# Kernel optimization log

Hardware: AMD Instinct MI355X
Metric: run time of the kernel (lower is better)

Reference implementation:

```python
import jax, jax.numpy as jnp
import numpy as np

MIN_DIST = 32  # minimum_extrema_distance from init_kwargs


def _extrema_mask(x):
    # x: [L]. Matches torch: dx padded with 0 on right (>0) and left (<=0);
    # sign = (1 - sign(x)).bool() is True iff x <= 0.
    dx = x[1:] - x[:-1]
    right = jnp.pad(dx, (0, 1)) > 0        # rising on the right
    left = jnp.pad(dx, (1, 0)) <= 0        # non-rising on the left
    neg = x <= 0
    valleys = right & left & neg
    peaks = (~right) & (~left) & (~neg)
    return valleys | peaks


def _suppress(x):
    # Greedy NMS-like suppression over one sample. x: [L]
    L = x.shape[0]
    e = _extrema_mask(x)
    # Sort ALL positions by |x| descending, with non-extrema pushed to the end
    key = jnp.where(e, jnp.abs(x), -jnp.inf)
    order = jnp.argsort(-key)              # candidate j -> original index order[j]
    valid = e[order]                       # which sorted candidates are real extrema
    idx = order                            # original positions, in sorted order

    def step(sec, i):
        # If candidate i not yet suppressed: suppress all candidates within
        # MIN_DIST of its position, then un-suppress itself.
        cond = jnp.logical_not(sec[i])
        window = (idx >= idx[i] - MIN_DIST) & (idx <= idx[i] + MIN_DIST)
        new_sec = jnp.where(cond, (sec | window).at[i].set(False), sec)
        return new_sec, None

    sec0 = jnp.logical_not(valid)          # non-extrema start suppressed
    sec, _ = jax.lax.scan(step, sec0, jnp.arange(L))
    primary_sorted = valid & jnp.logical_not(sec)
    # scatter back to original positions (order is a permutation)
    primary = jnp.zeros((L,), dtype=bool).at[order].set(primary_sorted)
    return jnp.where(primary, x, jnp.zeros_like(x))


def setup_inputs() -> dict:
    key = jax.random.key(0)
    input_ = jax.random.normal(key, (128, 1, 4096), dtype=jnp.float32)
    return {"input_": input_}


def reference(input_):
    x = input_[:, 0, :]                    # [B, L]
    out = jax.vmap(_suppress)(x)           # [B, L]
    return out[:, None, :]                 # [B, 1, L]
```

## Files before the change

kernel.cpp:

```cpp
#include <hip/hip_runtime.h>

#define L 4096
#define NT 256
#define C 16
#define NC (NT + 4)

typedef unsigned int u32;
typedef unsigned long long u64;

static __device__ __forceinline__ u32 umax(u32 a, u32 b) { return a > b ? a : b; }

__global__ __launch_bounds__(NT) void extrema_nms_kernel(const float* __restrict__ in,
                                                         float* __restrict__ out) {
    __shared__ u32 pfxT[C][NC];
    __shared__ u32 sfxT[C][NC];
    __shared__ u32 TA[NC];
    __shared__ u32 winmF[2 * NC];
    __shared__ int flagsF[2];

    const int tid = threadIdx.x;
    const int cc = tid + 2;
    const int base = tid * C;
    const float* xrow = in + (size_t)blockIdx.x * L;

    if (tid < 64) {
        int o = tid >> 2, c = tid & 3;
        int col = (c & 1) + ((c >> 1) ? (NT + 2) : 0);
        pfxT[o][col] = 0;
        sfxT[o][col] = 0;
    }
    if (tid < 2) { TA[tid] = 0; TA[NT + 2 + tid] = 0; }
    for (int w = tid; w < 2 * NC; w += NT) winmF[w] = 0;
    if (tid == 0) { flagsF[0] = 0; flagsF[1] = 0; }

    float xv[C];
    #pragma unroll
    for (int k = 0; k < C; k += 4) {
        float4 f = *reinterpret_cast<const float4*>(xrow + base + k);
        xv[k] = f.x; xv[k + 1] = f.y; xv[k + 2] = f.z; xv[k + 3] = f.w;
    }
    float xl = (base > 0) ? xrow[base - 1] : 0.0f;
    float xr = (base + C < L) ? xrow[base + C] : 0.0f;

    u32 key[C];
    #pragma unroll
    for (int o = 0; o < C; ++o) {
        int i = base + o;
        float xi = xv[o];
        float xp = (o == 0) ? xl : xv[o - 1];
        float xn = (o == C - 1) ? xr : xv[o + 1];
        bool right = (i < L - 1) && (xn > xi);
        bool left  = (i == 0) || (xi <= xp);
        bool neg   = (xi <= 0.0f);
        bool ext = (right && left && neg) || (!right && !left && !neg);
        key[o] = ext ? ((__float_as_uint(xi) & 0x7fffffffu) + 1u) : 0u;
    }

    u32 run = 0, om = 0;
    {
        u32 p = 0;
        #pragma unroll
        for (int o = 0; o < C; ++o) { p = umax(p, key[o]); pfxT[o][cc] = p; }
        TA[cc] = p;
        u32 s = 0;
        #pragma unroll
        for (int o = C - 1; o >= 0; --o) { s = umax(s, key[o]); sfxT[o][cc] = s; }
        #pragma unroll
        for (int o = 0; o < C; ++o) if (key[o] > run) { run = key[o]; om = (u32)o; }
    }
    u32 keptm = 0;
    __syncthreads();

    for (int r = 0; r < 200; ++r) {
        if (run) {
            u32 bL = umax(sfxT[om][cc - 2], TA[cc - 1]);
            u32 bR = umax(TA[cc + 1], pfxT[om][cc + 2]);
            u32 wm = (bL < run && bR <= run) ? (1u << om) : 0u;
            winmF[(r & 1) * NC + cc] = wm;
            if (wm) { keptm |= wm; flagsF[r & 1] = 1; }
        }
        __syncthreads();

        int go = flagsF[r & 1];
        const int pp = (r & 1) * NC;
        u32 m0 = winmF[pp + cc - 2], m1 = winmF[pp + cc - 1], m2 = winmF[pp + cc];
        u32 m3 = winmF[pp + cc + 1], m4 = winmF[pp + cc + 2];
        if (!go) break;
        if (tid == 0) flagsF[(r + 1) & 1] = 0;
        u64 W0 = (u64)(m0 & 0xffffu) | ((u64)(m1 & 0xffffu) << 16)
               | ((u64)(m2 & 0xffffu) << 32) | ((u64)(m3 & 0xffffu) << 48);
        u32 W1 = m4 & 0xffffu;
        u32 supmask = 0;
        if (W0) { int h0 = 63 - __clzll(W0); supmask = (u32)((2ULL << h0) - 1ULL); }
        if (W1) { int l1 = __ffs(W1) - 1;    supmask |= ~((1u << l1) - 1u); }
        supmask &= 0xffffu;
        if (run && supmask) {
            #pragma unroll
            for (int o = 0; o < C; ++o) if ((supmask >> o) & 1u) key[o] = 0;
            u32 p = 0;
            #pragma unroll
            for (int o = 0; o < C; ++o) { p = umax(p, key[o]); pfxT[o][cc] = p; }
            TA[cc] = p;
            u32 s = 0;
            #pragma unroll
            for (int o = C - 1; o >= 0; --o) { s = umax(s, key[o]); sfxT[o][cc] = s; }
            run = 0; om = 0;
            #pragma unroll
            for (int o = 0; o < C; ++o) if (key[o] > run) { run = key[o]; om = (u32)o; }
        }
        __syncthreads();
    }

    float* orow = out + (size_t)blockIdx.x * L;
    #pragma unroll
    for (int k = 0; k < C; k += 4) {
        float4 f;
        f.x = ((keptm >> (k + 0)) & 1u) ? xv[k + 0] : 0.0f;
        f.y = ((keptm >> (k + 1)) & 1u) ? xv[k + 1] : 0.0f;
        f.z = ((keptm >> (k + 2)) & 1u) ? xv[k + 2] : 0.0f;
        f.w = ((keptm >> (k + 3)) & 1u) ? xv[k + 3] : 0.0f;
        *reinterpret_cast<float4*>(orow + base + k) = f;
    }
}

extern "C" void kernel_launch(void* const* d_in, const int* in_sizes, int n_in,
                              void* d_out, int out_size, void* d_ws, size_t ws_size,
                              hipStream_t stream) {
    const float* in = (const float*)d_in[0];
    float* out = (float*)d_out;
    int rows = in_sizes[0] / L;
    extrema_nms_kernel<<<rows, NT, 0, stream>>>(in, out);
}
```

Baseline: 12.31 us.

## Transpose prefix/suffix tables to per-thread rows with vectorized shared stores

Moves the per-thread prefix and suffix max tables from column-major [C][NC] arrays to row-major per-thread rows padded to a stride of 20, so each thread writes its 16 values with four uint4 shared stores. The block total now lives in slot 16 of the prefix row instead of a separate array. It also fuses the argmax into the prefix scan, uses the thread's own window mask from a register instead of reloading it, and skips neighbour mask loads when the thread has no candidate. The padded stride is meant to limit bank conflicts, but neighbour reads at an index that varies per thread could still conflict.

```diff
diff --git a/kernel.cpp b/kernel.cpp
--- a/kernel.cpp
+++ b/kernel.cpp
@@ -4,6 +4,7 @@
 #define NT 256
 #define C 16
 #define NC (NT + 4)
+#define SS 20
 
 typedef unsigned int u32;
 typedef unsigned long long u64;
@@ -12,9 +13,8 @@
 
 __global__ __launch_bounds__(NT) void extrema_nms_kernel(const float* __restrict__ in,
                                                          float* __restrict__ out) {
-    __shared__ u32 pfxT[C][NC];
-    __shared__ u32 sfxT[C][NC];
-    __shared__ u32 TA[NC];
+    __shared__ u32 pfxS[NC * SS];
+    __shared__ u32 sfxS[NC * SS];
     __shared__ u32 winmF[2 * NC];
     __shared__ int flagsF[2];
 
@@ -23,14 +23,18 @@
     const int base = tid * C;
     const float* xrow = in + (size_t)blockIdx.x * L;
 
-    if (tid < 64) {
-        int o = tid >> 2, c = tid & 3;
-        int col = (c & 1) + ((c >> 1) ? (NT + 2) : 0);
-        pfxT[o][col] = 0;
-        sfxT[o][col] = 0;
+    if (tid < 4 * SS) {
+        int rsel = tid / SS;
+        int row = (rsel & 1) + ((rsel >> 1) ? (NT + 2) : 0);
+        int col = tid % SS;
+        pfxS[row * SS + col] = 0;
+        sfxS[row * SS + col] = 0;
     }
-    if (tid < 2) { TA[tid] = 0; TA[NT + 2 + tid] = 0; }
-    for (int w = tid; w < 2 * NC; w += NT) winmF[w] = 0;
+    if (tid < 4) {
+        int slot = (tid & 1) + ((tid >> 1) ? (NT + 2) : 0);
+        winmF[slot] = 0;
+        winmF[NC + slot] = 0;
+    }
     if (tid == 0) { flagsF[0] = 0; flagsF[1] = 0; }
 
     float xv[C];
@@ -56,57 +60,73 @@
         key[o] = ext ? ((__float_as_uint(xi) & 0x7fffffffu) + 1u) : 0u;
     }
 
-    u32 run = 0, om = 0;
+    u32 run, om;
     {
-        u32 p = 0;
+        u32 pf[C], sf[C];
+        u32 p = 0, nom = 0;
         #pragma unroll
-        for (int o = 0; o < C; ++o) { p = umax(p, key[o]); pfxT[o][cc] = p; }
-        TA[cc] = p;
+        for (int o = 0; o < C; ++o) { u32 k = key[o]; if (k > p) { p = k; nom = (u32)o; } pf[o] = p; }
         u32 s = 0;
         #pragma unroll
-        for (int o = C - 1; o >= 0; --o) { s = umax(s, key[o]); sfxT[o][cc] = s; }
+        for (int o = C - 1; o >= 0; --o) { s = umax(s, key[o]); sf[o] = s; }
+        u32* pr = &pfxS[cc * SS];
+        u32* sr = &sfxS[cc * SS];
         #pragma unroll
-        for (int o = 0; o < C; ++o) if (key[o] > run) { run = key[o]; om = (u32)o; }
+        for (int k4 = 0; k4 < C; k4 += 4) {
+            *reinterpret_cast<uint4*>(pr + k4) = make_uint4(pf[k4], pf[k4+1], pf[k4+2], pf[k4+3]);
+            *reinterpret_cast<uint4*>(sr + k4) = make_uint4(sf[k4], sf[k4+1], sf[k4+2], sf[k4+3]);
+        }
+        pr[16] = p;
+        run = p; om = nom;
     }
     u32 keptm = 0;
     __syncthreads();
 
     for (int r = 0; r < 200; ++r) {
+        u32 wm = 0;
         if (run) {
-            u32 bL = umax(sfxT[om][cc - 2], TA[cc - 1]);
-            u32 bR = umax(TA[cc + 1], pfxT[om][cc + 2]);
-            u32 wm = (bL < run && bR <= run) ? (1u << om) : 0u;
-            winmF[(r & 1) * NC + cc] = wm;
-            if (wm) { keptm |= wm; flagsF[r & 1] = 1; }
+            u32 bL = umax(sfxS[(cc - 2) * SS + om], pfxS[(cc - 1) * SS + 16]);
+            u32 bR = umax(pfxS[(cc + 1) * SS + 16], pfxS[(cc + 2) * SS + om]);
+            if (bL < run && bR <= run) wm = 1u << om;
         }
+        winmF[(r & 1) * NC + cc] = wm;
+        if (wm) { keptm |= wm; flagsF[r & 1] = 1; }
         __syncthreads();
 
         int go = flagsF[r & 1];
-        const int pp = (r & 1) * NC;
-        u32 m0 = winmF[pp + cc - 2], m1 = winmF[pp + cc - 1], m2 = winmF[pp + cc];
-        u32 m3 = winmF[pp + cc + 1], m4 = winmF[pp + cc + 2];
+        u32 m0 = 0, m1 = 0, m3 = 0, m4 = 0;
+        if (run) {
+            const int pp = (r & 1) * NC;
+            m0 = winmF[pp + cc - 2]; m1 = winmF[pp + cc - 1];
+            m3 = winmF[pp + cc + 1]; m4 = winmF[pp + cc + 2];
+        }
+        if (tid == 0) flagsF[(r + 1) & 1] = 0;
         if (!go) break;
-        if (tid == 0) flagsF[(r + 1) & 1] = 0;
-        u64 W0 = (u64)(m0 & 0xffffu) | ((u64)(m1 & 0xffffu) << 16)
-               | ((u64)(m2 & 0xffffu) << 32) | ((u64)(m3 & 0xffffu) << 48);
-        u32 W1 = m4 & 0xffffu;
+        u64 W0 = (u64)m0 | ((u64)m1 << 16) | ((u64)wm << 32) | ((u64)m3 << 48);
+        u32 W1 = m4;
         u32 supmask = 0;
-        if (W0) { int h0 = 63 - __clzll(W0); supmask = (u32)((2ULL << h0) - 1ULL); }
-        if (W1) { int l1 = __ffs(W1) - 1;    supmask |= ~((1u << l1) - 1u); }
+        if (W0) { int h0 = 63 - __clzll(W0); supmask = (h0 >= 15) ? 0xffffu : ((2u << h0) - 1u); }
+        if (W1) { int l1 = __ffs((int)W1) - 1; supmask |= ~((1u << l1) - 1u); }
         supmask &= 0xffffu;
         if (run && supmask) {
             #pragma unroll
-            for (int o = 0; o < C; ++o) if ((supmask >> o) & 1u) key[o] = 0;
-            u32 p = 0;
+            for (int o = 0; o < C; ++o) key[o] = ((supmask >> o) & 1u) ? 0u : key[o];
+            u32 pf[C], sf[C];
+            u32 p = 0, nom = 0;
             #pragma unroll
-            for (int o = 0; o < C; ++o) { p = umax(p, key[o]); pfxT[o][cc] = p; }
-            TA[cc] = p;
+            for (int o = 0; o < C; ++o) { u32 k = key[o]; if (k > p) { p = k; nom = (u32)o; } pf[o] = p; }
             u32 s = 0;
             #pragma unroll
-            for (int o = C - 1; o >= 0; --o) { s = umax(s, key[o]); sfxT[o][cc] = s; }
-            run = 0; om = 0;
+            for (int o = C - 1; o >= 0; --o) { s = umax(s, key[o]); sf[o] = s; }
+            u32* pr = &pfxS[cc * SS];
+            u32* sr = &sfxS[cc * SS];
             #pragma unroll
-            for (int o = 0; o < C; ++o) if (key[o] > run) { run = key[o]; om = (u32)o; }
+            for (int k4 = 0; k4 < C; k4 += 4) {
+                *reinterpret_cast<uint4*>(pr + k4) = make_uint4(pf[k4], pf[k4+1], pf[k4+2], pf[k4+3]);
+                *reinterpret_cast<uint4*>(sr + k4) = make_uint4(sf[k4], sf[k4+1], sf[k4+2], sf[k4+3]);
+            }
+            pr[16] = p;
+            run = p; om = nom;
         }
         __syncthreads();
     }
```

New measurement: 11.79 us (median of 2 runs). 4.2% less time.
